# Optimization experiments

Hardware: AMD Instinct MI355X
Metric: run time of the kernel (lower is better)

## Reference

```python
import jax, jax.numpy as jnp
import numpy as np

DIM = 1024
RANK = 16


def setup_inputs() -> dict:
    key = jax.random.key(0)
    ks = jax.random.split(key, 9)
    s = 0.02
    return {
        "x": jax.random.normal(ks[0], (2, 4096, DIM), dtype=jnp.float32),
        "W_qkv": jax.random.normal(ks[1], (3 * DIM, DIM), dtype=jnp.float32) * s,
        "b_qkv": jax.random.normal(ks[2], (3 * DIM,), dtype=jnp.float32) * s,
        "A_q": jax.random.normal(ks[3], (RANK, DIM), dtype=jnp.float32) * s,
        "B_q": jax.random.normal(ks[4], (DIM, RANK), dtype=jnp.float32) * s,
        "A_k": jax.random.normal(ks[5], (RANK, DIM), dtype=jnp.float32) * s,
        "B_k": jax.random.normal(ks[6], (DIM, RANK), dtype=jnp.float32) * s,
        "A_v": jax.random.normal(ks[7], (RANK, DIM), dtype=jnp.float32) * s,
        "B_v": jax.random.normal(ks[8], (DIM, RANK), dtype=jnp.float32) * s,
        "alpha": jnp.float32(0.5),
    }


def reference(x, W_qkv, b_qkv, A_q, B_q, A_k, B_k, A_v, B_v, alpha):
    # base fused QKV projection: [B, S, 3*dim]
    qkv = jnp.einsum("bsd,od->bso", x, W_qkv) + b_qkv
    # low-rank adapters: x @ A.T @ B.T, rank=16
    lora_q = jnp.einsum("bsr,dr->bsd", jnp.einsum("bsd,rd->bsr", x, A_q), B_q)
    lora_k = jnp.einsum("bsr,dr->bsd", jnp.einsum("bsd,rd->bsr", x, A_k), B_k)
    lora_v = jnp.einsum("bsr,dr->bsd", jnp.einsum("bsd,rd->bsr", x, A_v), B_v)
    # scaled add into q/k/v slices (concat order matches torch slice layout)
    delta = jnp.concatenate([lora_q, lora_k, lora_v], axis=-1)
    return qkv + alpha * delta
```

## Files before the change

### kernel.cpp

```cpp
#include <hip/hip_runtime.h>
#include <stdint.h>

#define DIM    1024
#define RANK   16
#define M_TOT  8192
#define N_TOT  3072
#define K_TOT  1024

#define BM 128
#define BN 128
#define BK 64

typedef __attribute__((ext_vector_type(8))) short  s8v;
typedef __attribute__((ext_vector_type(4))) float  f4v;

__device__ __forceinline__ unsigned short f2bf(float f) {
    union { float f; unsigned int u; } v; v.f = f;
    unsigned int u = v.u;
    u += 0x7FFFu + ((u >> 16) & 1u);
    return (unsigned short)(u >> 16);
}

__global__ void prep(const float4* __restrict__ x, ushort4* __restrict__ xb,
                     const float* __restrict__ W,
                     const float* __restrict__ Aq, const float* __restrict__ Bq,
                     const float* __restrict__ Ak, const float* __restrict__ Bk,
                     const float* __restrict__ Av, const float* __restrict__ Bv,
                     const float* __restrict__ alpha_p,
                     unsigned short* __restrict__ Wb) {
    const int tid = threadIdx.x;
    if (blockIdx.x < 8192) {
        int i = blockIdx.x * 256 + tid;
        float4 v = x[i];
        ushort4 o;
        o.x = f2bf(v.x); o.y = f2bf(v.y); o.z = f2bf(v.z); o.w = f2bf(v.w);
        xb[i] = o;
    } else {
        const int o    = blockIdx.x - 8192;
        const int sel  = o >> 10;
        const int orow = o & 1023;
        const float* Am = (sel == 0) ? Aq : (sel == 1) ? Ak : Av;
        const float* Bm = (sel == 0) ? Bq : (sel == 1) ? Bk : Bv;

        __shared__ float sb[RANK];
        if (tid < RANK) sb[tid] = alpha_p[0] * Bm[orow * RANK + tid];
        __syncthreads();

        for (int d = tid; d < DIM; d += 256) {
            float acc = W[o * DIM + d];
            #pragma unroll
            for (int r = 0; r < RANK; ++r)
                acc += sb[r] * Am[r * DIM + d];
            Wb[o * DIM + d] = f2bf(acc);
        }
    }
}

__global__ __launch_bounds__(256, 3)
void gemm_bt(const unsigned short* __restrict__ Xb,
             const unsigned short* __restrict__ Wb,
             const float* __restrict__ bias,
             float* __restrict__ out) {
    __shared__ __align__(16) unsigned short As[BM * BK];
    __shared__ __align__(16) unsigned short Bs[BN * BK];

    const int tid  = threadIdx.x;
    const int wave = tid >> 6;
    const int lane = tid & 63;
    const int l15  = lane & 15;
    const int lq   = lane >> 4;
    const int wr   = wave >> 1;
    const int wc   = wave & 1;

    const int bm = blockIdx.x;
    const int bn = blockIdx.y;

    const unsigned short* aptr[4];
    const unsigned short* bptr[4];
    unsigned short* alds[4];
    unsigned short* blds[4];
    #pragma unroll
    for (int u = 0; u < 4; ++u) {
        const int c   = wave * 4 + u;
        const int row = ((c >> 1) << 4) + l15;
        const int col = ((c & 1) << 5) + (lq << 3);
        aptr[u] = Xb + (size_t)(bm * BM + row) * K_TOT + col;
        bptr[u] = Wb + (size_t)(bn * BN + row) * K_TOT + col;
        alds[u] = &As[c * 512 + lane * 8];
        blds[u] = &Bs[c * 512 + lane * 8];
    }

    s8v areg[4], breg[4];
    #pragma unroll
    for (int u = 0; u < 4; ++u) {
        areg[u] = *(const s8v*)(aptr[u]);
        breg[u] = *(const s8v*)(bptr[u]);
    }

    f4v acc[4][4] = {};

    for (int kk = 0; kk < K_TOT; kk += BK) {
        __syncthreads();
        #pragma unroll
        for (int u = 0; u < 4; ++u) {
            *(s8v*)(alds[u]) = areg[u];
            *(s8v*)(blds[u]) = breg[u];
        }
        __syncthreads();

        const int kn = (kk + BK < K_TOT) ? (kk + BK) : 0;
        #pragma unroll
        for (int u = 0; u < 4; ++u) {
            areg[u] = *(const s8v*)(aptr[u] + kn);
            breg[u] = *(const s8v*)(bptr[u] + kn);
        }

        const s8v* Avp = (const s8v*)As;
        const s8v* Bvp = (const s8v*)Bs;
        #pragma unroll
        for (int t = 0; t < 2; ++t) {
            s8v af[4], bf[4];
            #pragma unroll
            for (int i = 0; i < 4; ++i) {
                const int ia = wr * 4 + i;
                const int jb = wc * 4 + i;
                af[i] = Avp[(ia * 2 + t) * 64 + lane];
                bf[i] = Bvp[(jb * 2 + t) * 64 + lane];
            }
            #pragma unroll
            for (int i = 0; i < 4; ++i)
                #pragma unroll
                for (int j = 0; j < 4; ++j)
                    acc[i][j] = __builtin_amdgcn_mfma_f32_16x16x32_bf16(
                        af[i], bf[j], acc[i][j], 0, 0, 0);
        }
    }

    const int col_base = bn * BN + wc * 64;
    const int row_base = bm * BM + wr * 64 + lq * 4;
    #pragma unroll
    for (int j = 0; j < 4; ++j) {
        const int col = col_base + j * 16 + l15;
        const float bv = bias[col];
        #pragma unroll
        for (int i = 0; i < 4; ++i) {
            const int row = row_base + i * 16;
            #pragma unroll
            for (int r = 0; r < 4; ++r)
                out[(size_t)(row + r) * N_TOT + col] = acc[i][j][r] + bv;
        }
    }
}

extern "C" void kernel_launch(void* const* d_in, const int* in_sizes, int n_in,
                              void* d_out, int out_size, void* d_ws, size_t ws_size,
                              hipStream_t stream) {
    const float* x     = (const float*)d_in[0];
    const float* W     = (const float*)d_in[1];
    const float* b     = (const float*)d_in[2];
    const float* Aq    = (const float*)d_in[3];
    const float* Bq    = (const float*)d_in[4];
    const float* Ak    = (const float*)d_in[5];
    const float* Bk    = (const float*)d_in[6];
    const float* Av    = (const float*)d_in[7];
    const float* Bv    = (const float*)d_in[8];
    const float* alpha = (const float*)d_in[9];
    float* out = (float*)d_out;

    unsigned short* xb = (unsigned short*)d_ws;
    unsigned short* Wb = (unsigned short*)((char*)d_ws + (size_t)M_TOT * K_TOT * 2);

    prep<<<8192 + N_TOT, 256, 0, stream>>>((const float4*)x, (ushort4*)xb,
                                           W, Aq, Bq, Ak, Bk, Av, Bv, alpha, Wb);

    dim3 grid(M_TOT / BM, N_TOT / BN);
    gemm_bt<<<grid, 256, 0, stream>>>(xb, Wb, b, out);
}
```

Measured before the change: 244.5 us.

## Load GEMM MFMA fragments directly from global memory, dropping LDS staging

The GEMM no longer stages A and B tiles in shared memory with barriers. Each wave now loads its own MFMA fragments straight from global memory, double-buffered in registers across two 32-wide k halves. This removes LDS traffic and the __syncthreads, but each wave reloads data that waves in other rows or columns of the block also need, so global/L2 traffic doubles and loads are 16-byte per lane with strided rows, which may coalesce poorly.

```diff
diff --git a/kernel.cpp b/kernel.cpp
--- a/kernel.cpp
+++ b/kernel.cpp
@@ -9,7 +9,6 @@
 
 #define BM 128
 #define BN 128
-#define BK 64
 
 typedef __attribute__((ext_vector_type(8))) short  s8v;
 typedef __attribute__((ext_vector_type(4))) float  f4v;
@@ -61,9 +60,6 @@
              const unsigned short* __restrict__ Wb,
              const float* __restrict__ bias,
              float* __restrict__ out) {
-    __shared__ __align__(16) unsigned short As[BM * BK];
-    __shared__ __align__(16) unsigned short Bs[BN * BK];
-
     const int tid  = threadIdx.x;
     const int wave = tid >> 6;
     const int lane = tid & 63;
@@ -75,65 +71,49 @@
     const int bm = blockIdx.x;
     const int bn = blockIdx.y;
 
-    const unsigned short* aptr[4];
-    const unsigned short* bptr[4];
-    unsigned short* alds[4];
-    unsigned short* blds[4];
+    const unsigned short* ap[4];
+    const unsigned short* bp[4];
     #pragma unroll
-    for (int u = 0; u < 4; ++u) {
-        const int c   = wave * 4 + u;
-        const int row = ((c >> 1) << 4) + l15;
-        const int col = ((c & 1) << 5) + (lq << 3);
-        aptr[u] = Xb + (size_t)(bm * BM + row) * K_TOT + col;
-        bptr[u] = Wb + (size_t)(bn * BN + row) * K_TOT + col;
-        alds[u] = &As[c * 512 + lane * 8];
-        blds[u] = &Bs[c * 512 + lane * 8];
+    for (int i = 0; i < 4; ++i) {
+        ap[i] = Xb + (size_t)(bm * BM + wr * 64 + i * 16 + l15) * K_TOT + lq * 8;
+        bp[i] = Wb + (size_t)(bn * BN + wc * 64 + i * 16 + l15) * K_TOT + lq * 8;
     }
 
-    s8v areg[4], breg[4];
+    s8v a0[4], b0[4], a1[4], b1[4];
     #pragma unroll
-    for (int u = 0; u < 4; ++u) {
-        areg[u] = *(const s8v*)(aptr[u]);
-        breg[u] = *(const s8v*)(bptr[u]);
+    for (int i = 0; i < 4; ++i) {
+        a0[i] = *(const s8v*)(ap[i]);
+        b0[i] = *(const s8v*)(bp[i]);
     }
 
     f4v acc[4][4] = {};
 
-    for (int kk = 0; kk < K_TOT; kk += BK) {
-        __syncthreads();
+    for (int kk = 0; kk < K_TOT; kk += 64) {
+        const int k1 = kk + 32;
         #pragma unroll
-        for (int u = 0; u < 4; ++u) {
-            *(s8v*)(alds[u]) = areg[u];
-            *(s8v*)(blds[u]) = breg[u];
+        for (int i = 0; i < 4; ++i) {
+            a1[i] = *(const s8v*)(ap[i] + k1);
+            b1[i] = *(const s8v*)(bp[i] + k1);
         }
-        __syncthreads();
+        #pragma unroll
+        for (int i = 0; i < 4; ++i)
+            #pragma unroll
+            for (int j = 0; j < 4; ++j)
+                acc[i][j] = __builtin_amdgcn_mfma_f32_16x16x32_bf16(
+                    a0[i], b0[j], acc[i][j], 0, 0, 0);
 
-        const int kn = (kk + BK < K_TOT) ? (kk + BK) : 0;
+        const int k2 = (kk + 64) & (K_TOT - 1);
         #pragma unroll
-        for (int u = 0; u < 4; ++u) {
-            areg[u] = *(const s8v*)(aptr[u] + kn);
-            breg[u] = *(const s8v*)(bptr[u] + kn);
+        for (int i = 0; i < 4; ++i) {
+            a0[i] = *(const s8v*)(ap[i] + k2);
+            b0[i] = *(const s8v*)(bp[i] + k2);
         }
-
-        const s8v* Avp = (const s8v*)As;
-        const s8v* Bvp = (const s8v*)Bs;
         #pragma unroll
-        for (int t = 0; t < 2; ++t) {
-            s8v af[4], bf[4];
+        for (int i = 0; i < 4; ++i)
             #pragma unroll
-            for (int i = 0; i < 4; ++i) {
-                const int ia = wr * 4 + i;
-                const int jb = wc * 4 + i;
-                af[i] = Avp[(ia * 2 + t) * 64 + lane];
-                bf[i] = Bvp[(jb * 2 + t) * 64 + lane];
-            }
-            #pragma unroll
-            for (int i = 0; i < 4; ++i)
-                #pragma unroll
-                for (int j = 0; j < 4; ++j)
-                    acc[i][j] = __builtin_amdgcn_mfma_f32_16x16x32_bf16(
-                        af[i], bf[j], acc[i][j], 0, 0, 0);
-        }
+            for (int j = 0; j < 4; ++j)
+                acc[i][j] = __builtin_amdgcn_mfma_f32_16x16x32_bf16(
+                    a1[i], b1[j], acc[i][j], 0, 0, 0);
     }
 
     const int col_base = bn * BN + wc * 64;
```

After: 325.8 us. 33.2% more time.
